# Performance work log

Measured on AMD Instinct MI355X. Metric: run time of the kernel, lower is better.

The kernel has to match this reference:

```python
import jax, jax.numpy as jnp
import numpy as np

N_EMBD = 1024
N_HEAD = 16
HEAD_DIM = N_EMBD // N_HEAD
B, T = 4, 1024
EPS = 1e-5


def _linear_params(key, fan_in, fan_out):
    kw, kb = jax.random.split(key)
    bound = 1.0 / np.sqrt(fan_in)
    W = jax.random.uniform(kw, (fan_in, fan_out), minval=-bound, maxval=bound, dtype=jnp.float32)
    b = jax.random.uniform(kb, (fan_out,), minval=-bound, maxval=bound, dtype=jnp.float32)
    return W, b


def setup_inputs() -> dict:
    key = jax.random.key(0)
    ks = jax.random.split(key, 8)
    x = jax.random.normal(ks[0], (B, T, N_EMBD), dtype=jnp.float32)
    Wq, bq = _linear_params(ks[1], N_EMBD, N_EMBD)
    Wk, bk = _linear_params(ks[2], N_EMBD, N_EMBD)
    Wv, bv = _linear_params(ks[3], N_EMBD, N_EMBD)
    Wp, bp = _linear_params(ks[4], N_EMBD, N_EMBD)
    W1, b1 = _linear_params(ks[5], N_EMBD, 4 * N_EMBD)
    W2, b2 = _linear_params(ks[6], 4 * N_EMBD, N_EMBD)
    g1 = jnp.ones((N_EMBD,), jnp.float32); be1 = jnp.zeros((N_EMBD,), jnp.float32)
    g2 = jnp.ones((N_EMBD,), jnp.float32); be2 = jnp.zeros((N_EMBD,), jnp.float32)
    return {"x": x, "Wq": Wq, "bq": bq, "Wk": Wk, "bk": bk, "Wv": Wv, "bv": bv,
            "Wp": Wp, "bp": bp, "W1": W1, "b1": b1, "W2": W2, "b2": b2,
            "g1": g1, "be1": be1, "g2": g2, "be2": be2}


def _layernorm(x, g, b):
    mu = jnp.mean(x, axis=-1, keepdims=True)
    var = jnp.mean(jnp.square(x - mu), axis=-1, keepdims=True)
    return (x - mu) * jax.lax.rsqrt(var + EPS) * g + b


def _attention(x, Wq, bq, Wk, bk, Wv, bv, Wp, bp):
    Bsz, Tt, C = x.shape
    def heads(W, b):
        return (x @ W + b).reshape(Bsz, Tt, N_HEAD, HEAD_DIM).transpose(0, 2, 1, 3)  # [B,H,T,d]
    q, k, v = heads(Wq, bq), heads(Wk, bk), heads(Wv, bv)
    scores = jnp.einsum('bhqd,bhkd->bhqk', q, k) / np.sqrt(HEAD_DIM).astype(np.float32)
    causal = jnp.tril(jnp.ones((Tt, Tt), dtype=bool))
    scores = jnp.where(causal, scores, -jnp.inf)
    attn = jax.nn.softmax(scores, axis=-1)
    out = jnp.einsum('bhqk,bhkd->bhqd', attn, v)  # [B,H,T,d]
    out = out.transpose(0, 2, 1, 3).reshape(Bsz, Tt, C)
    return out @ Wp + bp


def _ff(x, W1, b1, W2, b2):
    h = jax.nn.gelu(x @ W1 + b1, approximate=False)  # torch nn.GELU default = exact erf
    return h @ W2 + b2


def reference(x, Wq, bq, Wk, bk, Wv, bv, Wp, bp, W1, b1, W2, b2, g1, be1, g2, be2):
    x = x + _attention(_layernorm(x, g1, be1), Wq, bq, Wk, bk, Wv, bv, Wp, bp)
    x = x + _ff(_layernorm(x, g2, be2), W1, b1, W2, b2)
    return x
```

## Files before the change

kernel.cpp:

```cpp
#include <hip/hip_runtime.h>
#include <hip/hip_bf16.h>

typedef __attribute__((ext_vector_type(8))) __bf16 bf16x8;
typedef __attribute__((ext_vector_type(4))) float f32x4;
typedef __attribute__((ext_vector_type(4))) unsigned short u16x4;
typedef unsigned short u16;

#define AS3(p) ((__attribute__((address_space(3))) void*)(p))
#define AS1(p) ((const __attribute__((address_space(1))) void*)(p))

#define QSCALE 0.18033688011112042f

__device__ __forceinline__ u16 f2b(float f) {
    __hip_bfloat16 h = __float2bfloat16(f);
    return __builtin_bit_cast(u16, h);
}

__device__ __forceinline__ float gelu_exact(float v) {
    const float z = v * 0.70710678118654752f;
    const float a = fabsf(z);
    const float t = __builtin_amdgcn_rcpf(1.0f + 0.3275911f * a);
    float p = 1.061405429f;
    p = p * t - 1.453152027f;
    p = p * t + 1.421413741f;
    p = p * t - 0.284496736f;
    p = p * t + 0.254829592f;
    p = p * t;
    float erfv = 1.0f - p * __expf(-a * a);
    erfv = copysignf(erfv, z);
    return 0.5f * v * (1.0f + erfv);
}

__global__ __launch_bounds__(256) void transpose_w(
    const float* __restrict__ W, u16* __restrict__ WT, int K, int N)
{
    __shared__ u16 tile[32][33];
    const int tx = threadIdx.x & 31, ty = threadIdx.x >> 5;
    const int n0 = blockIdx.x * 32, k0 = blockIdx.y * 32;
    #pragma unroll
    for (int p = 0; p < 4; ++p)
        tile[ty + p * 8][tx] = f2b(W[(size_t)(k0 + ty + p * 8) * N + n0 + tx]);
    __syncthreads();
    #pragma unroll
    for (int p = 0; p < 4; ++p)
        WT[(size_t)(n0 + ty + p * 8) * K + k0 + tx] = tile[tx][ty + p * 8];
}

__global__ __launch_bounds__(256) void transpose_w4(
    const float* __restrict__ W0, const float* __restrict__ W1,
    const float* __restrict__ W2, const float* __restrict__ W3,
    u16* __restrict__ WTqkv, u16* __restrict__ WTp)
{
    __shared__ u16 tile[32][33];
    const int z = blockIdx.z;
    const float* W = (z == 0) ? W0 : (z == 1) ? W1 : (z == 2) ? W2 : W3;
    u16* dst = (z == 3) ? WTp : WTqkv + (size_t)z * 1024 * 1024;
    const int tx = threadIdx.x & 31, ty = threadIdx.x >> 5;
    const int n0 = blockIdx.x * 32, k0 = blockIdx.y * 32;
    #pragma unroll
    for (int p = 0; p < 4; ++p)
        tile[ty + p * 8][tx] = f2b(W[(size_t)(k0 + ty + p * 8) * 1024 + n0 + tx]);
    __syncthreads();
    #pragma unroll
    for (int p = 0; p < 4; ++p)
        dst[(size_t)(n0 + ty + p * 8) * 1024 + k0 + tx] = tile[tx][ty + p * 8];
}

__global__ __launch_bounds__(256) void ln_bf16(
    const float* __restrict__ xin, const float* __restrict__ gam,
    const float* __restrict__ bet, u16* __restrict__ yout)
{
    __shared__ float red[8];
    const int row = blockIdx.x, tid = threadIdx.x;
    float4 v = ((const float4*)(xin + (size_t)row * 1024))[tid];
    float s = v.x + v.y + v.z + v.w;
    #pragma unroll
    for (int o = 32; o > 0; o >>= 1) s += __shfl_xor(s, o, 64);
    if ((tid & 63) == 0) red[tid >> 6] = s;
    __syncthreads();
    const float mu = (red[0] + red[1] + red[2] + red[3]) * (1.f / 1024.f);
    const float dx = v.x - mu, dy = v.y - mu, dz = v.z - mu, dw = v.w - mu;
    float sq = dx * dx + dy * dy + dz * dz + dw * dw;
    #pragma unroll
    for (int o = 32; o > 0; o >>= 1) sq += __shfl_xor(sq, o, 64);
    if ((tid & 63) == 0) red[4 + (tid >> 6)] = sq;
    __syncthreads();
    const float var = (red[4] + red[5] + red[6] + red[7]) * (1.f / 1024.f);
    const float inv = rsqrtf(var + 1e-5f);
    const float4 G = ((const float4*)gam)[tid];
    const float4 Bt = ((const float4*)bet)[tid];
    u16x4 o;
    o[0] = f2b(dx * inv * G.x + Bt.x);
    o[1] = f2b(dy * inv * G.y + Bt.y);
    o[2] = f2b(dz * inv * G.z + Bt.z);
    o[3] = f2b(dw * inv * G.w + Bt.w);
    ((u16x4*)(yout + (size_t)row * 1024))[tid] = o;
}

__global__ __launch_bounds__(256) void reduce_ln(
    const float* __restrict__ p0, const float* __restrict__ p1,
    const float* __restrict__ bias, const float* __restrict__ resid,
    const float* __restrict__ gam, const float* __restrict__ bet,
    float* __restrict__ xout, u16* __restrict__ yout)
{
    __shared__ float red[8];
    const int row = blockIdx.x, tid = threadIdx.x;
    const size_t off = (size_t)row * 256 + tid;
    float4 a = ((const float4*)p0)[off];
    const float4 b = ((const float4*)p1)[off];
    const float4 r = ((const float4*)resid)[off];
    const float4 bs = ((const float4*)bias)[tid];
    a.x += b.x + r.x + bs.x; a.y += b.y + r.y + bs.y;
    a.z += b.z + r.z + bs.z; a.w += b.w + r.w + bs.w;
    ((float4*)xout)[off] = a;
    float s = a.x + a.y + a.z + a.w;
    #pragma unroll
    for (int o = 32; o > 0; o >>= 1) s += __shfl_xor(s, o, 64);
    if ((tid & 63) == 0) red[tid >> 6] = s;
    __syncthreads();
    const float mu = (red[0] + red[1] + red[2] + red[3]) * (1.f / 1024.f);
    const float dx = a.x - mu, dy = a.y - mu, dz = a.z - mu, dw = a.w - mu;
    float sq = dx * dx + dy * dy + dz * dz + dw * dw;
    #pragma unroll
    for (int o = 32; o > 0; o >>= 1) sq += __shfl_xor(sq, o, 64);
    if ((tid & 63) == 0) red[4 + (tid >> 6)] = sq;
    __syncthreads();
    const float var = (red[4] + red[5] + red[6] + red[7]) * (1.f / 1024.f);
    const float inv = rsqrtf(var + 1e-5f);
    const float4 G = ((const float4*)gam)[tid];
    const float4 Bt = ((const float4*)bet)[tid];
    u16x4 o;
    o[0] = f2b(dx * inv * G.x + Bt.x);
    o[1] = f2b(dy * inv * G.y + Bt.y);
    o[2] = f2b(dz * inv * G.z + Bt.z);
    o[3] = f2b(dw * inv * G.w + Bt.w);
    ((u16x4*)(yout + (size_t)row * 1024))[tid] = o;
}

__global__ __launch_bounds__(256) void reduce_add3(
    const float* __restrict__ p0, const float* __restrict__ p1,
    const float* __restrict__ p2, const float* __restrict__ bias,
    const float* __restrict__ resid, float* __restrict__ out)
{
    const size_t i = (size_t)blockIdx.x * 256 + threadIdx.x;
    float4 a = ((const float4*)p0)[i];
    const float4 b = ((const float4*)p1)[i];
    const float4 c = ((const float4*)p2)[i];
    const float4 r = ((const float4*)resid)[i];
    const float4 bs = ((const float4*)bias)[i & 255];
    a.x += b.x + c.x + r.x + bs.x; a.y += b.y + c.y + r.y + bs.y;
    a.z += b.z + c.z + r.z + bs.z; a.w += b.w + c.w + r.w + bs.w;
    ((float4*)out)[i] = a;
}

template <int MODE, int BM, int SK>
__global__ __launch_bounds__(256, (BM == 128 ? 3 : 2)) void gemm_bf16(
    const u16* __restrict__ A, const u16* __restrict__ BT,
    const float* __restrict__ b0, const float* __restrict__ b1,
    const float* __restrict__ b2,
    void* __restrict__ outp, int M, int N, int K)
{
    constexpr int WM = BM / 2;
    constexpr int MI = WM / 16;
    constexpr int NI = 4;
    constexpr int AJ = BM / 64;
    constexpr int AELEM = BM * 32;
    constexpr int BELEM = 128 * 32;
    __shared__ u16 Asm[3 * AELEM];
    __shared__ u16 Bsm[3 * BELEM];

    const int tid = threadIdx.x;
    const int lane = tid & 63, wid = tid >> 6;
    const int wm = wid >> 1, wn = wid & 1;
    const int g = lane >> 4, l16 = lane & 15;
    const int sx = (l16 >> 1) & 3;
    const int sslot = (lane & 3) ^ ((lane >> 3) & 3);

    const int nBN = N >> 7;
    const int per = (M / BM) * nBN;
    const int cpx = gridDim.x >> 3;
    const int wg = (blockIdx.x & 7) * cpx + (blockIdx.x >> 3);
    const int skid = (SK > 1) ? (wg / per) : 0;
    const int rem = wg - skid * per;
    const int bm0 = (rem / nBN) * BM, bn0 = (rem % nBN) * 128;

    const int tsteps = K >> 5;
    const int sbase = tsteps / SK, srem = tsteps % SK;
    const int nt = sbase + (skid < srem ? 1 : 0);
    const int kstart = (skid * sbase + (skid < srem ? skid : srem)) << 5;

    f32x4 acc[MI][NI] = {};

    const u16* aBase = A + (size_t)(bm0 + (lane >> 2)) * K + kstart + sslot * 8;
    const u16* bBase = BT + (size_t)(bn0 + (lane >> 2)) * K + kstart + sslot * 8;

    auto stage = [&](int kt, int buf) {
        u16* adst = Asm + buf * AELEM + lane * 8;
        u16* bdst = Bsm + buf * BELEM + lane * 8;
        #pragma unroll
        for (int j = 0; j < AJ; ++j) {
            const int ia = wid * AJ + j;
            __builtin_amdgcn_global_load_lds(AS1(aBase + (size_t)(ia * 16) * K + kt),
                                             AS3(adst + ia * 512), 16, 0, 0);
        }
        #pragma unroll
        for (int j = 0; j < 2; ++j) {
            const int ib = wid * 2 + j;
            __builtin_amdgcn_global_load_lds(AS1(bBase + (size_t)(ib * 16) * K + kt),
                                             AS3(bdst + ib * 512), 16, 0, 0);
        }
    };

    stage(0, 0);
    stage(32, 1);
    int cur = 0, pre = 2;

    for (int t = 0; t < nt; ++t) {
        if (t + 1 < nt) {
            if constexpr (BM == 256) asm volatile("s_waitcnt vmcnt(6)" ::: "memory");
            else                     asm volatile("s_waitcnt vmcnt(4)" ::: "memory");
        } else {
            asm volatile("s_waitcnt vmcnt(0)" ::: "memory");
        }
        __builtin_amdgcn_s_barrier();
        __builtin_amdgcn_sched_barrier(0);

        const u16* asrc = Asm + cur * AELEM;
        const u16* bsrc = Bsm + cur * BELEM;
        bf16x8 af[MI], bfr[NI];
        #pragma unroll
        for (int mi = 0; mi < MI; ++mi) {
            const int r = wm * WM + mi * 16 + l16;
            af[mi] = *(const bf16x8*)(asrc + r * 32 + ((g ^ sx) << 3));
        }
        #pragma unroll
        for (int ni = 0; ni < NI; ++ni) {
            const int c = wn * 64 + ni * 16 + l16;
            bfr[ni] = *(const bf16x8*)(bsrc + c * 32 + ((g ^ sx) << 3));
        }
        if (t + 2 < nt) stage((t + 2) * 32, pre);

        #pragma unroll
        for (int mi = 0; mi < MI; ++mi)
            #pragma unroll
            for (int ni = 0; ni < NI; ++ni)
                acc[mi][ni] = __builtin_amdgcn_mfma_f32_16x16x32_bf16(
                    af[mi], bfr[ni], acc[mi][ni], 0, 0, 0);

        pre = cur;
        cur = (cur == 2) ? 0 : cur + 1;
    }

    #pragma unroll
    for (int mi = 0; mi < MI; ++mi) {
        #pragma unroll
        for (int ni = 0; ni < NI; ++ni) {
            #pragma unroll
            for (int j = 0; j < 4; ++j) {
                const int m = bm0 + wm * WM + mi * 16 + g * 4 + j;
                const int n = bn0 + wn * 64 + ni * 16 + l16;
                float v = acc[mi][ni][j];
                if constexpr (MODE == 0) {
                    const float bias = (n < 1024) ? b0[n]
                                      : (n < 2048) ? b1[n - 1024] : b2[n - 2048];
                    float o = v + bias;
                    if (n < 1024) o *= QSCALE;
                    ((u16*)outp)[(size_t)m * N + n] = f2b(o);
                } else if constexpr (MODE == 2) {
                    ((u16*)outp)[(size_t)m * N + n] = f2b(gelu_exact(v + b0[n]));
                } else {
                    float* pout = (float*)(skid == 0 ? b0 : skid == 1 ? b1 : b2);
                    pout[(size_t)m * N + n] = v;
                }
            }
        }
    }
}

__global__ __launch_bounds__(256) void attn_fwd(
    const u16* __restrict__ qkv, u16* __restrict__ outp)
{
    __shared__ u16 Ksm[2][64 * 64];
    __shared__ u16 Vsm[2][64 * 64];
    __shared__ u16 Psm[4][16 * 64];
    const int tid = threadIdx.x, lane = tid & 63, w = tid >> 6;
    const int lin = blockIdx.y * 8 + blockIdx.x;
    const int xq = (lin >> 3) & 7;
    const int bh = (((lin >> 6) & 7) << 3) | (lin & 7);
    const int b = bh >> 4, h = bh & 15;
    const int g = lane >> 4, l16 = lane & 15;
    const int skv = tid >> 4;
    const int sd4 = (tid & 15) * 4;

    const u16* kvb = qkv + (size_t)(b * 1024) * 3072 + 1024 + h * 64;

    bf16x8 vones;
    #pragma unroll
    for (int e = 0; e < 8; ++e) vones[e] = __builtin_bit_cast(__bf16, (u16)0x3F80);

    u16x4 kreg[4], vreg[4];
    auto issue = [&](int kv0) {
        const u16* kb = kvb + (size_t)kv0 * 3072;
        #pragma unroll
        for (int i = 0; i < 4; ++i)
            kreg[i] = *(const u16x4*)(kb + (size_t)(skv + 16 * i) * 3072 + sd4);
        #pragma unroll
        for (int i = 0; i < 4; ++i)
            vreg[i] = *(const u16x4*)(kb + (size_t)(4 * skv + i) * 3072 + 1024 + sd4);
    };
    auto stage_lds = [&](int buf) {
        #pragma unroll
        for (int i = 0; i < 4; ++i) {
            const int row = skv + 16 * i;
            *(u16x4*)(&Ksm[buf][row * 64 + (sd4 ^ ((row & 7) << 3))]) = kreg[i];
        }
        #pragma unroll
        for (int j = 0; j < 4; ++j) {
            u16x4 t;
            t[0] = vreg[0][j]; t[1] = vreg[1][j];
            t[2] = vreg[2][j]; t[3] = vreg[3][j];
            const int row = sd4 + j;
            *(u16x4*)(&Vsm[buf][row * 64 + ((4 * skv) ^ ((row & 7) << 3))]) = t;
        }
    };

    #pragma unroll
    for (int half = 0; half < 2; ++half) {
        const int qt = half ? (15 - xq) : xq;
        const int q0 = qt * 64;

        bf16x8 qf0, qf1;
        {
            const u16* qp = qkv + (size_t)(b * 1024 + q0 + w * 16 + l16) * 3072
                            + h * 64 + g * 8;
            qf0 = *(const bf16x8*)qp;
            qf1 = *(const bf16x8*)(qp + 32);
        }
        float m_run[4] = {-1e30f, -1e30f, -1e30f, -1e30f};
        float l_run[4] = {0.f, 0.f, 0.f, 0.f};
        f32x4 oacc[4] = {};

        issue(0);
        __syncthreads();
        stage_lds(0);
        if (qt > 0) issue(64);
        __syncthreads();
        int cur = 0;

        for (int kvt = 0; kvt <= qt; ++kvt) {
            f32x4 s[4];
            __builtin_amdgcn_s_setprio(1);
            #pragma unroll
            for (int t = 0; t < 4; ++t) {
                const int r = t * 16 + l16;
                const int sw = (r & 7) << 3;
                const bf16x8 kf0 = *(const bf16x8*)(&Ksm[cur][r * 64 + ((g * 8) ^ sw)]);
                const bf16x8 kf1 = *(const bf16x8*)(&Ksm[cur][r * 64 + (((g + 4) * 8) ^ sw)]);
                f32x4 z = {};
                z = __builtin_amdgcn_mfma_f32_16x16x32_bf16(qf0, kf0, z, 0, 0, 0);
                z = __builtin_amdgcn_mfma_f32_16x16x32_bf16(qf1, kf1, z, 0, 0, 0);
                s[t] = z;
            }
            __builtin_amdgcn_s_setprio(0);
            if (kvt == qt) {
                #pragma unroll
                for (int t = 0; t < 4; ++t)
                    #pragma unroll
                    for (int j = 0; j < 4; ++j) {
                        const int qrow = q0 + w * 16 + g * 4 + j;
                        const int kvc = q0 + t * 16 + l16;
                        if (kvc > qrow) s[t][j] = -1e30f;
                    }
            }
            float mx[4] = {-1e30f, -1e30f, -1e30f, -1e30f};
            #pragma unroll
            for (int t = 0; t < 4; ++t)
                #pragma unroll
                for (int j = 0; j < 4; ++j)
                    mx[j] = fmaxf(mx[j], s[t][j]);
            #pragma unroll
            for (int o = 1; o < 16; o <<= 1)
                #pragma unroll
                for (int j = 0; j < 4; ++j)
                    mx[j] = fmaxf(mx[j], __shfl_xor(mx[j], o, 16));
            float alpha[4];
            #pragma unroll
            for (int j = 0; j < 4; ++j) {
                const float mn = fmaxf(m_run[j], mx[j]);
                alpha[j] = __builtin_amdgcn_exp2f(m_run[j] - mn);
                m_run[j] = mn;
            }
            #pragma unroll
            for (int t = 0; t < 4; ++t)
                #pragma unroll
                for (int j = 0; j < 4; ++j)
                    s[t][j] = __builtin_amdgcn_exp2f(s[t][j] - m_run[j]);
            #pragma unroll
            for (int t = 0; t < 4; ++t)
                #pragma unroll
                for (int j = 0; j < 4; ++j) {
                    const int row = g * 4 + j;
                    Psm[w][row * 64 + ((t * 16 + l16) ^ ((row & 7) << 3))] = f2b(s[t][j]);
                }
            const int psw = (l16 & 7) << 3;
            const bf16x8 pf0 = *(const bf16x8*)(&Psm[w][l16 * 64 + ((g * 8) ^ psw)]);
            const bf16x8 pf1 = *(const bf16x8*)(&Psm[w][l16 * 64 + (((g + 4) * 8) ^ psw)]);
            f32x4 sum = {};
            sum = __builtin_amdgcn_mfma_f32_16x16x32_bf16(pf0, vones, sum, 0, 0, 0);
            sum = __builtin_amdgcn_mfma_f32_16x16x32_bf16(pf1, vones, sum, 0, 0, 0);
            #pragma unroll
            for (int j = 0; j < 4; ++j)
                l_run[j] = l_run[j] * alpha[j] + sum[j];
            #pragma unroll
            for (int dt = 0; dt < 4; ++dt)
                #pragma unroll
                for (int j = 0; j < 4; ++j)
                    oacc[dt][j] *= alpha[j];
            __builtin_amdgcn_s_setprio(1);
            #pragma unroll
            for (int dt = 0; dt < 4; ++dt) {
                const int rv = dt * 16 + l16;
                const int sw = (rv & 7) << 3;
                const bf16x8 vf0 = *(const bf16x8*)(&Vsm[cur][rv * 64 + ((g * 8) ^ sw)]);
                const bf16x8 vf1 = *(const bf16x8*)(&Vsm[cur][rv * 64 + (((g + 4) * 8) ^ sw)]);
                oacc[dt] = __builtin_amdgcn_mfma_f32_16x16x32_bf16(pf0, vf0, oacc[dt], 0, 0, 0);
                oacc[dt] = __builtin_amdgcn_mfma_f32_16x16x32_bf16(pf1, vf1, oacc[dt], 0, 0, 0);
            }
            __builtin_amdgcn_s_setprio(0);
            if (kvt < qt) {
                stage_lds(cur ^ 1);
                if (kvt + 2 <= qt) issue((kvt + 2) * 64);
                __syncthreads();
                cur ^= 1;
            }
        }
        #pragma unroll
        for (int j = 0; j < 4; ++j) l_run[j] = __builtin_amdgcn_rcpf(l_run[j]);
        #pragma unroll
        for (int dt = 0; dt < 4; ++dt)
            #pragma unroll
            for (int j = 0; j < 4; ++j) {
                const int m = b * 1024 + q0 + w * 16 + g * 4 + j;
                const int col = h * 64 + dt * 16 + l16;
                outp[(size_t)m * 1024 + col] = f2b(oacc[dt][j] * l_run[j]);
            }
    }
}

extern "C" void kernel_launch(void* const* d_in, const int* in_sizes, int n_in,
                              void* d_out, int out_size, void* d_ws, size_t ws_size,
                              hipStream_t stream)
{
    const float* x   = (const float*)d_in[0];
    const float* Wq  = (const float*)d_in[1];
    const float* bq  = (const float*)d_in[2];
    const float* Wk  = (const float*)d_in[3];
    const float* bk  = (const float*)d_in[4];
    const float* Wv  = (const float*)d_in[5];
    const float* bv  = (const float*)d_in[6];
    const float* Wp  = (const float*)d_in[7];
    const float* bp  = (const float*)d_in[8];
    const float* W1  = (const float*)d_in[9];
    const float* b1  = (const float*)d_in[10];
    const float* W2  = (const float*)d_in[11];
    const float* b2  = (const float*)d_in[12];
    const float* g1  = (const float*)d_in[13];
    const float* be1 = (const float*)d_in[14];
    const float* g2  = (const float*)d_in[15];
    const float* be2 = (const float*)d_in[16];

    char* ws = (char*)d_ws;
    const size_t MB = 1024 * 1024;
    u16*   ln_buf = (u16*)(ws);
    u16*   qkv    = (u16*)(ws + 8 * MB);
    u16*   attn_o = (u16*)(ws + 32 * MB);
    float* x1     = (float*)(ws + 40 * MB);
    u16*   hbuf   = (u16*)(ws + 56 * MB);
    u16*   wqkvT  = (u16*)(ws + 88 * MB);
    u16*   wpT    = (u16*)(ws + 94 * MB);
    u16*   w1T    = (u16*)(ws + 96 * MB);
    u16*   w2T    = (u16*)(ws + 104 * MB);
    float* projP0 = (float*)(ws + 56 * MB);
    float* projP1 = (float*)(ws + 72 * MB);
    float* ff2P0  = (float*)(ws + 8 * MB);
    float* ff2P1  = (float*)(ws + 24 * MB);
    float* ff2P2  = (float*)(ws + 88 * MB);

    transpose_w4<<<dim3(32, 32, 4), 256, 0, stream>>>(Wq, Wk, Wv, Wp, wqkvT, wpT);
    transpose_w<<<dim3(128, 32), 256, 0, stream>>>(W1, w1T, 1024, 4096);
    transpose_w<<<dim3(32, 128), 256, 0, stream>>>(W2, w2T, 4096, 1024);

    ln_bf16<<<4096, 256, 0, stream>>>(x, g1, be1, ln_buf);
    gemm_bf16<0, 128, 1><<<768, 256, 0, stream>>>(
        ln_buf, wqkvT, bq, bk, bv, qkv, 4096, 3072, 1024);
    attn_fwd<<<dim3(8, 64), 256, 0, stream>>>(qkv, attn_o);
    gemm_bf16<3, 128, 2><<<512, 256, 0, stream>>>(
        attn_o, wpT, projP0, projP1, nullptr, nullptr, 4096, 1024, 1024);
    reduce_ln<<<4096, 256, 0, stream>>>(
        projP0, projP1, bp, x, g2, be2, x1, ln_buf);
    gemm_bf16<2, 256, 1><<<512, 256, 0, stream>>>(
        ln_buf, w1T, b1, nullptr, nullptr, hbuf, 4096, 4096, 1024);
    gemm_bf16<3, 128, 3><<<768, 256, 0, stream>>>(
        hbuf, w2T, ff2P0, ff2P1, ff2P2, nullptr, 4096, 1024, 4096);
    reduce_add3<<<4096, 256, 0, stream>>>(
        ff2P0, ff2P1, ff2P2, b2, x1, (float*)d_out);
}
```

Measured before the change: 215.9 us.

## Replace split-K GEMMs with narrow-N tiles and fused bias-residual epilogue

Removes split-K from the projection and FF2 GEMMs. Each output tile now has a narrower N width (64) and runs the full K loop, writing bias plus residual directly in the epilogue. This drops the fp32 partial-sum buffers and the separate reduce kernels (reduce_ln, reduce_add3). The second layernorm becomes a plain ln_bf16 on x1. The trade-off is a smaller BN tile with lower MFMA reuse per load and a longer serial K loop on the FF2 GEMM (K=4096 with only 512 blocks), and the launch bounds for BM=128 drop from 3 to 2 waves.

```diff
diff --git a/kernel.cpp b/kernel.cpp
--- a/kernel.cpp
+++ b/kernel.cpp
@@ -97,64 +97,8 @@
     ((u16x4*)(yout + (size_t)row * 1024))[tid] = o;
 }
 
-__global__ __launch_bounds__(256) void reduce_ln(
-    const float* __restrict__ p0, const float* __restrict__ p1,
-    const float* __restrict__ bias, const float* __restrict__ resid,
-    const float* __restrict__ gam, const float* __restrict__ bet,
-    float* __restrict__ xout, u16* __restrict__ yout)
-{
-    __shared__ float red[8];
-    const int row = blockIdx.x, tid = threadIdx.x;
-    const size_t off = (size_t)row * 256 + tid;
-    float4 a = ((const float4*)p0)[off];
-    const float4 b = ((const float4*)p1)[off];
-    const float4 r = ((const float4*)resid)[off];
-    const float4 bs = ((const float4*)bias)[tid];
-    a.x += b.x + r.x + bs.x; a.y += b.y + r.y + bs.y;
-    a.z += b.z + r.z + bs.z; a.w += b.w + r.w + bs.w;
-    ((float4*)xout)[off] = a;
-    float s = a.x + a.y + a.z + a.w;
-    #pragma unroll
-    for (int o = 32; o > 0; o >>= 1) s += __shfl_xor(s, o, 64);
-    if ((tid & 63) == 0) red[tid >> 6] = s;
-    __syncthreads();
-    const float mu = (red[0] + red[1] + red[2] + red[3]) * (1.f / 1024.f);
-    const float dx = a.x - mu, dy = a.y - mu, dz = a.z - mu, dw = a.w - mu;
-    float sq = dx * dx + dy * dy + dz * dz + dw * dw;
-    #pragma unroll
-    for (int o = 32; o > 0; o >>= 1) sq += __shfl_xor(sq, o, 64);
-    if ((tid & 63) == 0) red[4 + (tid >> 6)] = sq;
-    __syncthreads();
-    const float var = (red[4] + red[5] + red[6] + red[7]) * (1.f / 1024.f);
-    const float inv = rsqrtf(var + 1e-5f);
-    const float4 G = ((const float4*)gam)[tid];
-    const float4 Bt = ((const float4*)bet)[tid];
-    u16x4 o;
-    o[0] = f2b(dx * inv * G.x + Bt.x);
-    o[1] = f2b(dy * inv * G.y + Bt.y);
-    o[2] = f2b(dz * inv * G.z + Bt.z);
-    o[3] = f2b(dw * inv * G.w + Bt.w);
-    ((u16x4*)(yout + (size_t)row * 1024))[tid] = o;
-}
-
-__global__ __launch_bounds__(256) void reduce_add3(
-    const float* __restrict__ p0, const float* __restrict__ p1,
-    const float* __restrict__ p2, const float* __restrict__ bias,
-    const float* __restrict__ resid, float* __restrict__ out)
-{
-    const size_t i = (size_t)blockIdx.x * 256 + threadIdx.x;
-    float4 a = ((const float4*)p0)[i];
-    const float4 b = ((const float4*)p1)[i];
-    const float4 c = ((const float4*)p2)[i];
-    const float4 r = ((const float4*)resid)[i];
-    const float4 bs = ((const float4*)bias)[i & 255];
-    a.x += b.x + c.x + r.x + bs.x; a.y += b.y + c.y + r.y + bs.y;
-    a.z += b.z + c.z + r.z + bs.z; a.w += b.w + c.w + r.w + bs.w;
-    ((float4*)out)[i] = a;
-}
-
-template <int MODE, int BM, int SK>
-__global__ __launch_bounds__(256, (BM == 128 ? 3 : 2)) void gemm_bf16(
+template <int MODE, int BM, int BN>
+__global__ __launch_bounds__(256, 2) void gemm_bf16(
     const u16* __restrict__ A, const u16* __restrict__ BT,
     const float* __restrict__ b0, const float* __restrict__ b1,
     const float* __restrict__ b2,
@@ -162,10 +106,12 @@
 {
     constexpr int WM = BM / 2;
     constexpr int MI = WM / 16;
-    constexpr int NI = 4;
+    constexpr int NI = BN / 32;
     constexpr int AJ = BM / 64;
+    constexpr int BJ = BN / 64;
+    constexpr int LPS = AJ + BJ;
     constexpr int AELEM = BM * 32;
-    constexpr int BELEM = 128 * 32;
+    constexpr int BELEM = BN * 32;
     __shared__ u16 Asm[3 * AELEM];
     __shared__ u16 Bsm[3 * BELEM];
 
@@ -176,23 +122,15 @@
     const int sx = (l16 >> 1) & 3;
     const int sslot = (lane & 3) ^ ((lane >> 3) & 3);
 
-    const int nBN = N >> 7;
-    const int per = (M / BM) * nBN;
+    const int nBN = N / BN;
     const int cpx = gridDim.x >> 3;
     const int wg = (blockIdx.x & 7) * cpx + (blockIdx.x >> 3);
-    const int skid = (SK > 1) ? (wg / per) : 0;
-    const int rem = wg - skid * per;
-    const int bm0 = (rem / nBN) * BM, bn0 = (rem % nBN) * 128;
-
-    const int tsteps = K >> 5;
-    const int sbase = tsteps / SK, srem = tsteps % SK;
-    const int nt = sbase + (skid < srem ? 1 : 0);
-    const int kstart = (skid * sbase + (skid < srem ? skid : srem)) << 5;
+    const int bm0 = (wg / nBN) * BM, bn0 = (wg % nBN) * BN;
 
     f32x4 acc[MI][NI] = {};
 
-    const u16* aBase = A + (size_t)(bm0 + (lane >> 2)) * K + kstart + sslot * 8;
-    const u16* bBase = BT + (size_t)(bn0 + (lane >> 2)) * K + kstart + sslot * 8;
+    const u16* aBase = A + (size_t)(bm0 + (lane >> 2)) * K + sslot * 8;
+    const u16* bBase = BT + (size_t)(bn0 + (lane >> 2)) * K + sslot * 8;
 
     auto stage = [&](int kt, int buf) {
         u16* adst = Asm + buf * AELEM + lane * 8;
@@ -204,21 +142,23 @@
                                              AS3(adst + ia * 512), 16, 0, 0);
         }
         #pragma unroll
-        for (int j = 0; j < 2; ++j) {
-            const int ib = wid * 2 + j;
+        for (int j = 0; j < BJ; ++j) {
+            const int ib = wid * BJ + j;
             __builtin_amdgcn_global_load_lds(AS1(bBase + (size_t)(ib * 16) * K + kt),
                                              AS3(bdst + ib * 512), 16, 0, 0);
         }
     };
 
+    const int nt = K >> 5;
     stage(0, 0);
     stage(32, 1);
     int cur = 0, pre = 2;
 
     for (int t = 0; t < nt; ++t) {
         if (t + 1 < nt) {
-            if constexpr (BM == 256) asm volatile("s_waitcnt vmcnt(6)" ::: "memory");
-            else                     asm volatile("s_waitcnt vmcnt(4)" ::: "memory");
+            if constexpr (LPS == 6)      asm volatile("s_waitcnt vmcnt(6)" ::: "memory");
+            else if constexpr (LPS == 4) asm volatile("s_waitcnt vmcnt(4)" ::: "memory");
+            else                         asm volatile("s_waitcnt vmcnt(3)" ::: "memory");
         } else {
             asm volatile("s_waitcnt vmcnt(0)" ::: "memory");
         }
@@ -235,7 +175,7 @@
         }
         #pragma unroll
         for (int ni = 0; ni < NI; ++ni) {
-            const int c = wn * 64 + ni * 16 + l16;
+            const int c = wn * (BN / 2) + ni * 16 + l16;
             bfr[ni] = *(const bf16x8*)(bsrc + c * 32 + ((g ^ sx) << 3));
         }
         if (t + 2 < nt) stage((t + 2) * 32, pre);
@@ -258,7 +198,7 @@
             #pragma unroll
             for (int j = 0; j < 4; ++j) {
                 const int m = bm0 + wm * WM + mi * 16 + g * 4 + j;
-                const int n = bn0 + wn * 64 + ni * 16 + l16;
+                const int n = bn0 + wn * (BN / 2) + ni * 16 + l16;
                 float v = acc[mi][ni][j];
                 if constexpr (MODE == 0) {
                     const float bias = (n < 1024) ? b0[n]
@@ -266,11 +206,11 @@
                     float o = v + bias;
                     if (n < 1024) o *= QSCALE;
                     ((u16*)outp)[(size_t)m * N + n] = f2b(o);
-                } else if constexpr (MODE == 2) {
+                } else if constexpr (MODE == 1) {
+                    ((float*)outp)[(size_t)m * N + n] =
+                        v + b0[n] + b1[(size_t)m * N + n];
+                } else {
                     ((u16*)outp)[(size_t)m * N + n] = f2b(gelu_exact(v + b0[n]));
-                } else {
-                    float* pout = (float*)(skid == 0 ? b0 : skid == 1 ? b1 : b2);
-                    pout[(size_t)m * N + n] = v;
                 }
             }
         }
@@ -480,28 +420,20 @@
     u16*   wpT    = (u16*)(ws + 94 * MB);
     u16*   w1T    = (u16*)(ws + 96 * MB);
     u16*   w2T    = (u16*)(ws + 104 * MB);
-    float* projP0 = (float*)(ws + 56 * MB);
-    float* projP1 = (float*)(ws + 72 * MB);
-    float* ff2P0  = (float*)(ws + 8 * MB);
-    float* ff2P1  = (float*)(ws + 24 * MB);
-    float* ff2P2  = (float*)(ws + 88 * MB);
 
     transpose_w4<<<dim3(32, 32, 4), 256, 0, stream>>>(Wq, Wk, Wv, Wp, wqkvT, wpT);
     transpose_w<<<dim3(128, 32), 256, 0, stream>>>(W1, w1T, 1024, 4096);
     transpose_w<<<dim3(32, 128), 256, 0, stream>>>(W2, w2T, 4096, 1024);
 
     ln_bf16<<<4096, 256, 0, stream>>>(x, g1, be1, ln_buf);
-    gemm_bf16<0, 128, 1><<<768, 256, 0, stream>>>(
+    gemm_bf16<0, 128, 128><<<768, 256, 0, stream>>>(
         ln_buf, wqkvT, bq, bk, bv, qkv, 4096, 3072, 1024);
     attn_fwd<<<dim3(8, 64), 256, 0, stream>>>(qkv, attn_o);
-    gemm_bf16<3, 128, 2><<<512, 256, 0, stream>>>(
-        attn_o, wpT, projP0, projP1, nullptr, nullptr, 4096, 1024, 1024);
-    reduce_ln<<<4096, 256, 0, stream>>>(
-        projP0, projP1, bp, x, g2, be2, x1, ln_buf);
-    gemm_bf16<2, 256, 1><<<512, 256, 0, stream>>>(
+    gemm_bf16<1, 128, 64><<<512, 256, 0, stream>>>(
+        attn_o, wpT, bp, x, nullptr, x1, 4096, 1024, 1024);
+    ln_bf16<<<4096, 256, 0, stream>>>(x1, g2, be2, ln_buf);
+    gemm_bf16<2, 256, 128><<<512, 256, 0, stream>>>(
         ln_buf, w1T, b1, nullptr, nullptr, hbuf, 4096, 4096, 1024);
-    gemm_bf16<3, 128, 3><<<768, 256, 0, stream>>>(
-        hbuf, w2T, ff2P0, ff2P1, ff2P2, nullptr, 4096, 1024, 4096);
-    reduce_add3<<<4096, 256, 0, stream>>>(
-        ff2P0, ff2P1, ff2P2, b2, x1, (float*)d_out);
-}
+    gemm_bf16<1, 128, 64><<<512, 256, 0, stream>>>(
+        hbuf, w2T, b2, x1, nullptr, (float*)d_out, 4096, 1024, 4096);
+}
```

Result: faster. 209.5 us (-3.0%).
